# Optimization experiments

Measured on AMD Instinct MI355X. Metric: run time of the kernel, lower is better.

The kernel has to match this reference:

```python
import jax, jax.numpy as jnp
import numpy as np
from jax import lax

B, N, C = 4, 3072, 512
SAMPLE_RATIO = 0.25
CLUSTER_NUM = int(np.ceil(N * SAMPLE_RATIO))  # 768, static (mask=None, no 'r')
K = 5  # self.k, since k <= cluster_num


def setup_inputs() -> dict:
    key = jax.random.key(0)
    k1, = jax.random.split(key, 1)
    x = jax.random.normal(k1, (B, N, C), dtype=jnp.float32)
    # idx_token starts as identity mapping per batch (standard TCFormer init)
    idx_token = jnp.tile(jnp.arange(N, dtype=jnp.int32)[None, :], (B, 1))
    agg_weight = jnp.ones((B, N, 1), dtype=jnp.float32)
    return {"x": x, "idx_token": idx_token, "agg_weight": agg_weight}


def _cluster_dpc_knn(x):
    # runs under no_grad in torch -> stop_gradient here
    xs = lax.stop_gradient(x).astype(jnp.float32)
    sq = jnp.sum(xs * xs, axis=-1)  # [B,N]
    d2 = sq[:, :, None] + sq[:, None, :] - 2.0 * jnp.einsum('bnc,bmc->bnm', xs, xs)
    dist = jnp.sqrt(jnp.maximum(d2, 0.0)) / jnp.sqrt(jnp.float32(C))  # cdist / C**0.5
    # k nearest (smallest) distances
    neg_nearest, _ = lax.top_k(-dist, K)
    dist_nearest = -neg_nearest  # [B,N,K]
    density = jnp.exp(-jnp.mean(dist_nearest ** 2, axis=-1))
    density = density + jax.random.uniform(jax.random.key(42), density.shape, dtype=density.dtype) * 1e-6
    mask = (density[:, None, :] > density[:, :, None]).astype(x.dtype)  # [B,N,N]
    dist_max = jnp.max(dist.reshape(B, -1), axis=-1)[:, None, None]
    dist_min = jnp.min(dist * mask + dist_max * (1.0 - mask), axis=-1)  # [B,N]
    score = dist_min * density
    _, index_down = lax.top_k(score, CLUSTER_NUM)  # [B,cluster]
    # gather rows of dist at cluster centers, assign each token to nearest center
    dmat = jnp.take_along_axis(dist, index_down[:, :, None], axis=1)  # [B,cluster,N]
    idx_cluster = jnp.argmin(dmat, axis=1).astype(jnp.int32)  # [B,N]
    # force centers to map to their own cluster id
    idx_cluster = idx_cluster.at[jnp.arange(B)[:, None], index_down].set(
        jnp.broadcast_to(jnp.arange(CLUSTER_NUM, dtype=jnp.int32)[None, :], (B, CLUSTER_NUM)))
    return idx_cluster


def reference(x, idx_token, agg_weight):
    idx_cluster = _cluster_dpc_knn(x)
    # merge_tokens
    token_weight = jnp.ones((B, N, 1), dtype=x.dtype)
    idx = idx_cluster + jnp.arange(B, dtype=jnp.int32)[:, None] * CLUSTER_NUM  # [B,N]
    idx_flat = idx.reshape(-1)
    all_weight = jax.ops.segment_sum(token_weight.reshape(-1), idx_flat,
                                     num_segments=B * CLUSTER_NUM) + 1e-6  # [B*cluster]
    norm_weight = token_weight / all_weight[idx_flat].reshape(B, N, 1)  # [B,N,1]
    x_merged = jax.ops.segment_sum((x * norm_weight).reshape(B * N, C), idx_flat,
                                   num_segments=B * CLUSTER_NUM).reshape(B, CLUSTER_NUM, C)
    idx_token_new = jnp.take_along_axis(idx_cluster, idx_token, axis=1)  # [B,N]
    weight_t = jnp.take_along_axis(norm_weight, idx_token[:, :, None], axis=1)  # [B,N,1]
    agg_weight_new = agg_weight * weight_t
    return x_merged, agg_weight_new, idx_token_new, idx_cluster
```

## Files before the change

### kernel.cpp

```cpp
#include <hip/hip_runtime.h>
#include <math.h>
#include <float.h>

constexpr int B  = 4;
constexpr int N  = 3072;
constexpr int C  = 512;
constexpr int CL = 768;

typedef unsigned short u16;
typedef __attribute__((ext_vector_type(8))) short s16x8;
typedef __attribute__((ext_vector_type(4))) float f32x4;

__device__ __forceinline__ unsigned rotl32(unsigned v, int d) { return (v << d) | (v >> (32 - d)); }

__device__ inline void threefry2x32(unsigned k0, unsigned k1, unsigned c0, unsigned c1,
                                    unsigned& o0, unsigned& o1) {
  unsigned ks0 = k0, ks1 = k1, ks2 = 0x1BD11BDAu ^ k0 ^ k1;
  unsigned x0 = c0 + ks0, x1 = c1 + ks1;
#define TF_RND(r) { x0 += x1; x1 = rotl32(x1, (r)); x1 ^= x0; }
  TF_RND(13) TF_RND(15) TF_RND(26) TF_RND(6)  x0 += ks1; x1 += ks2 + 1u;
  TF_RND(17) TF_RND(29) TF_RND(16) TF_RND(24) x0 += ks2; x1 += ks0 + 2u;
  TF_RND(13) TF_RND(15) TF_RND(26) TF_RND(6)  x0 += ks0; x1 += ks1 + 3u;
  TF_RND(17) TF_RND(29) TF_RND(16) TF_RND(24) x0 += ks1; x1 += ks2 + 4u;
  TF_RND(13) TF_RND(15) TF_RND(26) TF_RND(6)  x0 += ks2; x1 += ks0 + 5u;
#undef TF_RND
  o0 = x0; o1 = x1;
}

__device__ inline float jax_uniform_bn(int f) {
  constexpr int HALF = (B * N) / 2;
  unsigned o0, o1, bits;
  if (f < HALF) { threefry2x32(0u, 42u, (unsigned)f, (unsigned)(f + HALF), o0, o1); bits = o0; }
  else          { threefry2x32(0u, 42u, (unsigned)(f - HALF), (unsigned)f, o0, o1); bits = o1; }
  return __uint_as_float((bits >> 9) | 0x3f800000u) - 1.0f;
}

__global__ void k_init(int* counts, unsigned long long* packed) {
  int g = blockIdx.x * 256 + threadIdx.x;
  packed[g] = ~0ull;
  if (g < B * CL) counts[g] = 0;
}

__global__ __launch_bounds__(64) void k_sq(const float* __restrict__ x, float* __restrict__ sq) {
  int row = blockIdx.x;
  int lane = threadIdx.x;
  const float* xr = x + (size_t)row * C;
  float s = 0.f;
  for (int c = lane * 4; c < C; c += 256) {
    float4 v = *(const float4*)(xr + c);
    s += v.x * v.x + v.y * v.y + v.z * v.z + v.w * v.w;
  }
  for (int o = 32; o > 0; o >>= 1) s += __shfl_down(s, o, 64);
  if (lane == 0) sq[row] = s;
}

__device__ __forceinline__ u16 bf16rn(float f) {
  unsigned u = __float_as_uint(f);
  unsigned r = u + 0x7FFFu + ((u >> 16) & 1u);
  return (u16)(r >> 16);
}
__device__ __forceinline__ float bf16tof(u16 h) {
  return __uint_as_float(((unsigned)h) << 16);
}

__global__ void k_split(const float* __restrict__ x, u16* __restrict__ xhi, u16* __restrict__ xlo) {
  int g = (blockIdx.x * 256 + threadIdx.x) * 4;
  float4 v = *(const float4*)(x + g);
  u16 h0 = bf16rn(v.x), h1 = bf16rn(v.y), h2 = bf16rn(v.z), h3 = bf16rn(v.w);
  u16 l0 = bf16rn(v.x - bf16tof(h0));
  u16 l1 = bf16rn(v.y - bf16tof(h1));
  u16 l2 = bf16rn(v.z - bf16tof(h2));
  u16 l3 = bf16rn(v.w - bf16tof(h3));
  uint2 hp, lp;
  hp.x = (unsigned)h0 | ((unsigned)h1 << 16); hp.y = (unsigned)h2 | ((unsigned)h3 << 16);
  lp.x = (unsigned)l0 | ((unsigned)l1 << 16); lp.y = (unsigned)l2 | ((unsigned)l3 << 16);
  *(uint2*)(xhi + g) = hp;
  *(uint2*)(xlo + g) = lp;
}

__device__ __forceinline__ void ins5b(float t[5], float v) {
  float c = v;
  float n;
  n = fminf(t[0], c); c = fmaxf(t[0], c); t[0] = n;
  n = fminf(t[1], c); c = fmaxf(t[1], c); t[1] = n;
  n = fminf(t[2], c); c = fmaxf(t[2], c); t[2] = n;
  n = fminf(t[3], c); c = fmaxf(t[3], c); t[3] = n;
  t[4] = fminf(t[4], c);
}

constexpr int NT3 = N / 128;
constexpr int NTILE3 = NT3 * (NT3 + 1) / 2;

__global__ __launch_bounds__(256) void k_distm(const u16* __restrict__ xhi, const u16* __restrict__ xlo,
                                               const float* __restrict__ sq,
                                               float* __restrict__ distbuf,
                                               float* __restrict__ part5, int b0) {
  constexpr int ASTR = 40;
  __shared__ __align__(16) char smem[40960];
  u16* sAh = (u16*)smem;
  u16* sAl = sAh + 128 * ASTR;
  u16* sBh = sAl + 128 * ASTR;
  u16* sBl = sBh + 128 * ASTR;

  int bl = blockIdx.y, b = b0 + bl;
  int idx = blockIdx.x;
  int ti = 0, rem = idx;
  while (rem >= NT3 - ti) { rem -= NT3 - ti; ++ti; }
  int tj = ti + rem;
  int i0 = ti * 128, j0 = tj * 128;
  bool do_mirror = (ti != tj);

  const float* sqb = sq + (size_t)b * N;
  float* dist = distbuf + (size_t)bl * N * N;

  int tid = threadIdx.x;
  int srow = tid >> 1, shalf = (tid & 1) * 16;
  const u16* gAh = xhi + ((size_t)b * N + i0 + srow) * C + shalf;
  const u16* gAl = xlo + ((size_t)b * N + i0 + srow) * C + shalf;
  const u16* gBh = xhi + ((size_t)b * N + j0 + srow) * C + shalf;
  const u16* gBl = xlo + ((size_t)b * N + j0 + srow) * C + shalf;
  int wofs = srow * ASTR + shalf;

  int lane = tid & 63, w = tid >> 6;
  int wr = (w >> 1) * 64, wc = (w & 1) * 64;
  int l15 = lane & 15, l4 = lane >> 4;

  f32x4 acc[4][4];
#pragma unroll
  for (int rt = 0; rt < 4; ++rt)
#pragma unroll
    for (int ct = 0; ct < 4; ++ct)
#pragma unroll
      for (int e = 0; e < 4; ++e) acc[rt][ct][e] = 0.f;

  uint4 p0 = *(const uint4*)gAh, p1 = *(const uint4*)(gAh + 8);
  uint4 p2 = *(const uint4*)gAl, p3 = *(const uint4*)(gAl + 8);
  uint4 p4 = *(const uint4*)gBh, p5 = *(const uint4*)(gBh + 8);
  uint4 p6 = *(const uint4*)gBl, p7 = *(const uint4*)(gBl + 8);

  for (int k0 = 0; k0 < C; k0 += 32) {
    *(uint4*)&sAh[wofs] = p0; *(uint4*)&sAh[wofs + 8] = p1;
    *(uint4*)&sAl[wofs] = p2; *(uint4*)&sAl[wofs + 8] = p3;
    *(uint4*)&sBh[wofs] = p4; *(uint4*)&sBh[wofs + 8] = p5;
    *(uint4*)&sBl[wofs] = p6; *(uint4*)&sBl[wofs + 8] = p7;
    __syncthreads();
    int kn = k0 + 32;
    if (kn < C) {
      p0 = *(const uint4*)(gAh + kn); p1 = *(const uint4*)(gAh + kn + 8);
      p2 = *(const uint4*)(gAl + kn); p3 = *(const uint4*)(gAl + kn + 8);
      p4 = *(const uint4*)(gBh + kn); p5 = *(const uint4*)(gBh + kn + 8);
      p6 = *(const uint4*)(gBl + kn); p7 = *(const uint4*)(gBl + kn + 8);
    }
    s16x8 ah[4], al[4];
#pragma unroll
    for (int rt = 0; rt < 4; ++rt) {
      int ro = (wr + rt * 16 + l15) * ASTR + l4 * 8;
      ah[rt] = *(const s16x8*)&sAh[ro];
      al[rt] = *(const s16x8*)&sAl[ro];
    }
#pragma unroll
    for (int ct = 0; ct < 4; ++ct) {
      int co = (wc + ct * 16 + l15) * ASTR + l4 * 8;
      s16x8 bh = *(const s16x8*)&sBh[co];
      s16x8 bl = *(const s16x8*)&sBl[co];
#pragma unroll
      for (int rt = 0; rt < 4; ++rt) {
        acc[rt][ct] = __builtin_amdgcn_mfma_f32_16x16x32_bf16(ah[rt], bh, acc[rt][ct], 0, 0, 0);
        acc[rt][ct] = __builtin_amdgcn_mfma_f32_16x16x32_bf16(ah[rt], bl, acc[rt][ct], 0, 0, 0);
        acc[rt][ct] = __builtin_amdgcn_mfma_f32_16x16x32_bf16(al[rt], bh, acc[rt][ct], 0, 0, 0);
      }
    }
    __syncthreads();
  }

  const float SQC = 22.627416997969522f;
  float sqi[4][4], sqj[4];
#pragma unroll
  for (int rt = 0; rt < 4; ++rt)
#pragma unroll
    for (int r = 0; r < 4; ++r) sqi[rt][r] = sqb[i0 + wr + rt * 16 + l4 * 4 + r];
#pragma unroll
  for (int ct = 0; ct < 4; ++ct) sqj[ct] = sqb[j0 + wc + ct * 16 + l15];

#pragma unroll
  for (int rt = 0; rt < 4; ++rt)
#pragma unroll
    for (int ct = 0; ct < 4; ++ct)
#pragma unroll
      for (int r = 0; r < 4; ++r) {
        float d2 = fmaxf(sqi[rt][r] + sqj[ct] - 2.0f * acc[rt][ct][r], 0.0f);
        acc[rt][ct][r] = sqrtf(d2) / SQC;
      }

  constexpr int TSTR = 76;
  float* sT = (float*)smem + w * (32 * TSTR);

  float t5A[5] = {FLT_MAX, FLT_MAX, FLT_MAX, FLT_MAX, FLT_MAX};
  float mxA = 0.f;

#pragma unroll
  for (int p = 0; p < 2; ++p) {
#pragma unroll
    for (int cth = 0; cth < 2; ++cth) {
      int ct = p * 2 + cth;
      int cl = cth * 16 + l15;
#pragma unroll
      for (int rt = 0; rt < 4; ++rt)
#pragma unroll
        for (int r = 0; r < 4; ++r)
          sT[cl * TSTR + rt * 16 + l4 * 4 + r] = acc[rt][ct][r];
    }
    {
      int g4 = lane & 7, rbase = lane >> 3;
#pragma unroll
      for (int it = 0; it < 8; ++it) {
        int rl = it * 8 + rbase;
        float4 v = make_float4(sT[(4 * g4 + 0) * TSTR + rl],
                               sT[(4 * g4 + 1) * TSTR + rl],
                               sT[(4 * g4 + 2) * TSTR + rl],
                               sT[(4 * g4 + 3) * TSTR + rl]);
        *(float4*)(dist + (size_t)(i0 + wr + rl) * N + j0 + wc + p * 32 + 4 * g4) = v;
      }
    }
    if (do_mirror) {
      int cg = lane >> 4, rq = lane & 15;
#pragma unroll
      for (int cc = 0; cc < 8; ++cc) {
        int c = cc * 4 + cg;
        float4 v = *(const float4*)&sT[c * TSTR + rq * 4];
        *(float4*)(dist + (size_t)(j0 + wc + p * 32 + c) * N + i0 + wr + rq * 4) = v;
      }
    }
    for (int c = 0; c < 32; ++c) {
      float v = sT[c * TSTR + lane];
      mxA = fmaxf(mxA, v);
      ins5b(t5A, v);
    }
    if (do_mirror) {
      int cl = lane & 31, half = lane >> 5;
      float t5B[5] = {FLT_MAX, FLT_MAX, FLT_MAX, FLT_MAX, FLT_MAX};
      float mxB = 0.f;
      for (int k = 0; k < 32; ++k) {
        float v = sT[cl * TSTR + half * 32 + k];
        mxB = fmaxf(mxB, v);
        ins5b(t5B, v);
      }
      mxB = fmaxf(mxB, __shfl_xor(mxB, 32, 64));
      float o0 = __shfl_xor(t5B[0], 32, 64);
      float o1 = __shfl_xor(t5B[1], 32, 64);
      float o2 = __shfl_xor(t5B[2], 32, 64);
      float o3 = __shfl_xor(t5B[3], 32, 64);
      float o4 = __shfl_xor(t5B[4], 32, 64);
      ins5b(t5B, o0); ins5b(t5B, o1); ins5b(t5B, o2); ins5b(t5B, o3); ins5b(t5B, o4);
      if (half == 0) {
        int rowB = j0 + wc + p * 32 + cl;
        int slotB = ti * 2 + (wr >> 6);
        float* dst = part5 + (((size_t)bl * 48 + slotB) * 6) * N + rowB;
        dst[0] = t5B[0]; dst[(size_t)N] = t5B[1]; dst[2 * (size_t)N] = t5B[2];
        dst[3 * (size_t)N] = t5B[3]; dst[4 * (size_t)N] = t5B[4]; dst[5 * (size_t)N] = mxB;
      }
    }
  }
  {
    int rowA = i0 + wr + lane;
    int slotA = tj * 2 + (wc >> 6);
    float* dst = part5 + (((size_t)bl * 48 + slotA) * 6) * N + rowA;
    dst[0] = t5A[0]; dst[(size_t)N] = t5A[1]; dst[2 * (size_t)N] = t5A[2];
    dst[3 * (size_t)N] = t5A[3]; dst[4 * (size_t)N] = t5A[4]; dst[5 * (size_t)N] = mxA;
  }
}

__global__ __launch_bounds__(256) void k_dens(const float* __restrict__ part5,
                                              float* __restrict__ density,
                                              float* __restrict__ rowmax, int b0) {
  int g = blockIdx.x * 256 + threadIdx.x;
  int bl = g / N, r = g % N;
  int b = b0 + bl;
  const float* base = part5 + (size_t)bl * 48 * 6 * N + r;
  float t5[5] = {FLT_MAX, FLT_MAX, FLT_MAX, FLT_MAX, FLT_MAX};
  float mx = 0.f;
  for (int s = 0; s < 48; ++s) {
    const float* sp = base + (size_t)s * 6 * N;
    ins5b(t5, sp[0]);
    ins5b(t5, sp[(size_t)N]);
    ins5b(t5, sp[2 * (size_t)N]);
    ins5b(t5, sp[3 * (size_t)N]);
    ins5b(t5, sp[4 * (size_t)N]);
    mx = fmaxf(mx, sp[5 * (size_t)N]);
  }
  float sum = t5[0] * t5[0] + t5[1] * t5[1] + t5[2] * t5[2] + t5[3] * t5[3] + t5[4] * t5[4];
  density[b * N + r] = expf(-(sum / 5.0f)) + jax_uniform_bn(b * N + r) * 1e-6f;
  rowmax[b * N + r] = mx;
}

__global__ __launch_bounds__(1024) void k_dmax(const float* __restrict__ rowmax,
                                               float* __restrict__ distmax) {
  __shared__ float red[16];
  int b = blockIdx.x;
  int tid = threadIdx.x;
  const float* rb = rowmax + (size_t)b * N;
  float mx = 0.f;
  for (int j = tid; j < N; j += 1024) mx = fmaxf(mx, rb[j]);
#pragma unroll
  for (int m = 1; m < 64; m <<= 1) mx = fmaxf(mx, __shfl_xor(mx, m, 64));
  if ((tid & 63) == 0) red[tid >> 6] = mx;
  __syncthreads();
  if (tid == 0) {
    float r = red[0];
#pragma unroll
    for (int q = 1; q < 16; ++q) r = fmaxf(r, red[q]);
    distmax[b] = r;
  }
}

__global__ __launch_bounds__(256) void k_maskmin(const float* __restrict__ distbuf,
                                                 const float* __restrict__ density,
                                                 const float* __restrict__ distmax,
                                                 float* __restrict__ score, int b0) {
  __shared__ float sd[N];
  int tid = threadIdx.x;
  int wv = tid >> 6, lane = tid & 63;
  int i = blockIdx.x * 4 + wv;
  int bl = blockIdx.y, b = b0 + bl;
  const float* db = density + (size_t)b * N;
  for (int j = tid * 4; j < N; j += 1024) *(float4*)(sd + j) = *(const float4*)(db + j);
  __syncthreads();
  float di = sd[i];
  float dmax = distmax[b];
  const float* row = distbuf + ((size_t)bl * N + i) * N;
  float mn = dmax;
#pragma unroll
  for (int it = 0; it < N / 256; ++it) {
    int j = it * 256 + lane * 4;
    float4 v = *(const float4*)(row + j);
    float4 d = *(const float4*)(sd + j);
    mn = fminf(mn, (d.x > di) ? v.x : dmax);
    mn = fminf(mn, (d.y > di) ? v.y : dmax);
    mn = fminf(mn, (d.z > di) ? v.z : dmax);
    mn = fminf(mn, (d.w > di) ? v.w : dmax);
  }
#pragma unroll
  for (int m = 1; m < 64; m <<= 1) mn = fminf(mn, __shfl_xor(mn, m, 64));
  if (lane == 0) score[b * N + i] = mn * di;
}

__global__ __launch_bounds__(256) void k_rank(const float* __restrict__ score,
                                              int* __restrict__ index_down,
                                              int* __restrict__ rank, int b0) {
  __shared__ float ssc[N];
  int tid = threadIdx.x;
  int wv = tid >> 6, lane = tid & 63;
  int i = blockIdx.x * 4 + wv;
  int b = b0 + blockIdx.y;
  const float* sb = score + (size_t)b * N;
  for (int j = tid * 4; j < N; j += 1024) *(float4*)(ssc + j) = *(const float4*)(sb + j);
  __syncthreads();
  float si = ssc[i];
  int cnt = 0;
#pragma unroll
  for (int it = 0; it < N / 256; ++it) {
    int j = it * 256 + lane * 4;
    float4 v = *(const float4*)(ssc + j);
    cnt += (v.x > si) || (v.x == si && (j + 0) < i);
    cnt += (v.y > si) || (v.y == si && (j + 1) < i);
    cnt += (v.z > si) || (v.z == si && (j + 2) < i);
    cnt += (v.w > si) || (v.w == si && (j + 3) < i);
  }
#pragma unroll
  for (int m = 1; m < 64; m <<= 1) cnt += __shfl_xor(cnt, m, 64);
  if (lane == 0) {
    rank[b * N + i] = (cnt < CL) ? cnt : -1;
    if (cnt < CL) index_down[b * CL + cnt] = i;
  }
}

__global__ __launch_bounds__(256) void k_assign_part(const float* __restrict__ distbuf,
                                                     const int* __restrict__ index_down,
                                                     unsigned long long* __restrict__ packed, int b0) {
  constexpr int RCH = CL / 8;
  __shared__ int sid[RCH];
  int bl = blockIdx.z, b = b0 + bl;
  int r0 = blockIdx.y * RCH;
  int tid = threadIdx.x;
  for (int r = tid; r < RCH; r += 256) sid[r] = index_down[b * CL + r0 + r];
  __syncthreads();
  int j = blockIdx.x * 256 + tid;
  const float* base = distbuf + (size_t)bl * N * N;
  float best = FLT_MAX; int bestr = 0;
#pragma unroll 8
  for (int r = 0; r < RCH; ++r) {
    float d = base[(size_t)sid[r] * N + j];
    if (d < best) { best = d; bestr = r0 + r; }
  }
  unsigned long long key = ((unsigned long long)__float_as_uint(best) << 32) | (unsigned)bestr;
  atomicMin(&packed[b * N + j], key);
}

__global__ void k_assign_fin2(const unsigned long long* __restrict__ packed,
                              const int* __restrict__ rank,
                              int* __restrict__ idx_cluster, int* __restrict__ counts) {
  int g = blockIdx.x * 256 + threadIdx.x;
  int b = g / N;
  int r = rank[g];
  int cl = (r >= 0) ? r : (int)(unsigned)(packed[g] & 0xffffffffull);
  idx_cluster[g] = cl;
  atomicAdd(&counts[b * CL + cl], 1);
}

__global__ __launch_bounds__(1024) void k_scan(const int* __restrict__ counts,
                                               int* __restrict__ offsets, int* __restrict__ cursor) {
  constexpr int T = B * CL;
  __shared__ int sm[T];
  int tid = threadIdx.x;
  for (int p = tid; p < T; p += 1024) sm[p] = counts[p];
  __syncthreads();
  for (int off = 1; off < T; off <<= 1) {
    int v[3]; int n = 0;
    for (int p = tid; p < T; p += 1024) { v[n++] = (p >= off) ? sm[p - off] : 0; }
    __syncthreads();
    n = 0;
    for (int p = tid; p < T; p += 1024) { sm[p] += v[n++]; }
    __syncthreads();
  }
  for (int p = tid; p < T; p += 1024) {
    int e = sm[p] - counts[p];
    offsets[p] = e; cursor[p] = e;
  }
}

__global__ void k_fill(const int* __restrict__ idx_cluster, int* __restrict__ cursor,
                       int* __restrict__ members) {
  int g = blockIdx.x * 256 + threadIdx.x;
  int b = g / N, i = g % N;
  int seg = b * CL + idx_cluster[g];
  int pos = atomicAdd(&cursor[seg], 1);
  members[pos] = i;
}

__global__ __launch_bounds__(128) void k_gather(const float* __restrict__ x, const int* __restrict__ members,
                                                const int* __restrict__ offsets, const int* __restrict__ counts,
                                                float* __restrict__ out0) {
  int seg = blockIdx.x;
  int b = seg / CL;
  int cnt = counts[seg], off = offsets[seg];
  float nw = 1.0f / ((float)cnt + 1e-6f);
  int c = threadIdx.x * 4;
  const float* xb = x + (size_t)b * N * C;
  float4 acc = make_float4(0.f, 0.f, 0.f, 0.f);
  for (int m = 0; m < cnt; ++m) {
    int tok = members[off + m];
    float4 v = *(const float4*)(xb + (size_t)tok * C + c);
    acc.x += v.x * nw; acc.y += v.y * nw; acc.z += v.z * nw; acc.w += v.w * nw;
  }
  *(float4*)(out0 + (size_t)seg * C + c) = acc;
}

__global__ void k_final(const float* __restrict__ agg_weight, const int* __restrict__ idx_token,
                        const int* __restrict__ idx_cluster, const int* __restrict__ counts,
                        float* __restrict__ out1, float* __restrict__ out2, float* __restrict__ out3) {
  int g = blockIdx.x * 256 + threadIdx.x;
  int b = g / N;
  int it = idx_token[g];
  int clt = idx_cluster[b * N + it];
  float nwt = 1.0f / ((float)counts[b * CL + clt] + 1e-6f);
  out1[g] = agg_weight[g] * nwt;
  out2[g] = (float)clt;
  out3[g] = (float)idx_cluster[g];
}

extern "C" void kernel_launch(void* const* d_in, const int* in_sizes, int n_in,
                              void* d_out, int out_size, void* d_ws, size_t ws_size,
                              hipStream_t stream) {
  const float* x          = (const float*)d_in[0];
  const int*   idx_token  = (const int*)d_in[1];
  const float* agg_weight = (const float*)d_in[2];

  float* out0 = (float*)d_out;
  float* out1 = out0 + (size_t)B * CL * C;
  float* out2 = out1 + (size_t)B * N;
  float* out3 = out2 + (size_t)B * N;

  char* w = (char*)d_ws;
  auto carve = [&](size_t bytes) { char* p = w; w += (bytes + 255) & ~(size_t)255; return p; };
  float*    sq         = (float*)carve((size_t)B * N * 4);
  float*    density    = (float*)carve((size_t)B * N * 4);
  float*    score      = (float*)carve((size_t)B * N * 4);
  float*    rowmax     = (float*)carve((size_t)B * N * 4);
  float*    distmax    = (float*)carve((size_t)B * 4);
  int*      index_down = (int*)carve((size_t)B * CL * 4);
  int*      rank       = (int*)carve((size_t)B * N * 4);
  int*      idx_clus   = (int*)carve((size_t)B * N * 4);
  int*      counts     = (int*)carve((size_t)B * CL * 4);
  int*      offsets    = (int*)carve((size_t)B * CL * 4);
  int*      cursor     = (int*)carve((size_t)B * CL * 4);
  int*      members    = (int*)carve((size_t)B * N * 4);
  unsigned long long* packed = (unsigned long long*)carve((size_t)B * N * 8);
  u16*      xhi        = (u16*)carve((size_t)B * N * C * 2);
  u16*      xlo        = (u16*)carve((size_t)B * N * C * 2);
  float*    part5      = (float*)carve((size_t)B * 48 * 6 * N * 4);
  size_t used = (size_t)(w - (char*)d_ws);
  size_t per  = (size_t)N * N * 4;
  int nb_max = (ws_size > used) ? (int)((ws_size - used) / per) : 0;
  if (nb_max < 1) nb_max = 1;
  if (nb_max > B) nb_max = B;
  float* distbuf = (float*)w;

  k_init<<<(B * N) / 256, 256, 0, stream>>>(counts, packed);
  k_sq<<<B * N, 64, 0, stream>>>(x, sq);
  k_split<<<(B * N * C) / 1024, 256, 0, stream>>>(x, xhi, xlo);

  for (int b0 = 0; b0 < B; b0 += nb_max) {
    int nb = (B - b0 < nb_max) ? (B - b0) : nb_max;
    k_distm<<<dim3(NTILE3, nb), 256, 0, stream>>>(xhi, xlo, sq, distbuf, part5, b0);
    k_dens<<<(nb * N) / 256, 256, 0, stream>>>(part5, density, rowmax, b0);
    k_dmax<<<nb, 1024, 0, stream>>>(rowmax + (size_t)b0 * N, distmax + b0);
    k_maskmin<<<dim3(N / 4, nb), 256, 0, stream>>>(distbuf, density, distmax, score, b0);
    k_rank<<<dim3(N / 4, nb), 256, 0, stream>>>(score, index_down, rank, b0);
    k_assign_part<<<dim3(N / 256, 8, nb), 256, 0, stream>>>(distbuf, index_down, packed, b0);
  }

  k_assign_fin2<<<(B * N) / 256, 256, 0, stream>>>(packed, rank, idx_clus, counts);
  k_scan<<<1, 1024, 0, stream>>>(counts, offsets, cursor);
  k_fill<<<(B * N) / 256, 256, 0, stream>>>(idx_clus, cursor, members);
  k_gather<<<B * CL, 128, 0, stream>>>(x, members, offsets, counts, out0);
  k_final<<<(B * N) / 256, 256, 0, stream>>>(agg_weight, idx_token, idx_clus, counts, out1, out2, out3);
}
```

Before: 307.1 us.

## Recompute distances via GEMM instead of materializing the full distance matrix

The full B×N×N fp32 distance matrix is no longer written to global memory. Masked-min and cluster-assignment stages now recompute distances with split-bf16 MFMA GEMMs: a second symmetric GEMM pass does the density-masked min, and a gathered center×token GEMM does the argmin. The sq, split and init kernels are fused into one prep kernel, and the per-batch chunking loop is removed. This trades roughly 150MB of dist writes and rereads for extra tensor-core work. It also adds partial-min buffers and an extra reduction kernel.

```diff
diff --git a/kernel.cpp b/kernel.cpp
--- a/kernel.cpp
+++ b/kernel.cpp
@@ -35,47 +35,45 @@
   return __uint_as_float((bits >> 9) | 0x3f800000u) - 1.0f;
 }
 
-__global__ void k_init(int* counts, unsigned long long* packed) {
-  int g = blockIdx.x * 256 + threadIdx.x;
-  packed[g] = ~0ull;
-  if (g < B * CL) counts[g] = 0;
-}
-
-__global__ __launch_bounds__(64) void k_sq(const float* __restrict__ x, float* __restrict__ sq) {
+__device__ __forceinline__ u16 bf16rn(float f) {
+  unsigned u = __float_as_uint(f);
+  unsigned r = u + 0x7FFFu + ((u >> 16) & 1u);
+  return (u16)(r >> 16);
+}
+__device__ __forceinline__ float bf16tof(u16 h) {
+  return __uint_as_float(((unsigned)h) << 16);
+}
+
+__global__ __launch_bounds__(64) void k_prep(const float* __restrict__ x, float* __restrict__ sq,
+                                             u16* __restrict__ xhi, u16* __restrict__ xlo,
+                                             int* __restrict__ counts,
+                                             unsigned long long* __restrict__ packed) {
   int row = blockIdx.x;
   int lane = threadIdx.x;
   const float* xr = x + (size_t)row * C;
+  u16* hr = xhi + (size_t)row * C;
+  u16* lr = xlo + (size_t)row * C;
   float s = 0.f;
   for (int c = lane * 4; c < C; c += 256) {
     float4 v = *(const float4*)(xr + c);
     s += v.x * v.x + v.y * v.y + v.z * v.z + v.w * v.w;
+    u16 h0 = bf16rn(v.x), h1 = bf16rn(v.y), h2 = bf16rn(v.z), h3 = bf16rn(v.w);
+    u16 l0 = bf16rn(v.x - bf16tof(h0));
+    u16 l1 = bf16rn(v.y - bf16tof(h1));
+    u16 l2 = bf16rn(v.z - bf16tof(h2));
+    u16 l3 = bf16rn(v.w - bf16tof(h3));
+    uint2 hp, lp;
+    hp.x = (unsigned)h0 | ((unsigned)h1 << 16); hp.y = (unsigned)h2 | ((unsigned)h3 << 16);
+    lp.x = (unsigned)l0 | ((unsigned)l1 << 16); lp.y = (unsigned)l2 | ((unsigned)l3 << 16);
+    *(uint2*)(hr + c) = hp;
+    *(uint2*)(lr + c) = lp;
   }
   for (int o = 32; o > 0; o >>= 1) s += __shfl_down(s, o, 64);
-  if (lane == 0) sq[row] = s;
-}
-
-__device__ __forceinline__ u16 bf16rn(float f) {
-  unsigned u = __float_as_uint(f);
-  unsigned r = u + 0x7FFFu + ((u >> 16) & 1u);
-  return (u16)(r >> 16);
-}
-__device__ __forceinline__ float bf16tof(u16 h) {
-  return __uint_as_float(((unsigned)h) << 16);
-}
-
-__global__ void k_split(const float* __restrict__ x, u16* __restrict__ xhi, u16* __restrict__ xlo) {
-  int g = (blockIdx.x * 256 + threadIdx.x) * 4;
-  float4 v = *(const float4*)(x + g);
-  u16 h0 = bf16rn(v.x), h1 = bf16rn(v.y), h2 = bf16rn(v.z), h3 = bf16rn(v.w);
-  u16 l0 = bf16rn(v.x - bf16tof(h0));
-  u16 l1 = bf16rn(v.y - bf16tof(h1));
-  u16 l2 = bf16rn(v.z - bf16tof(h2));
-  u16 l3 = bf16rn(v.w - bf16tof(h3));
-  uint2 hp, lp;
-  hp.x = (unsigned)h0 | ((unsigned)h1 << 16); hp.y = (unsigned)h2 | ((unsigned)h3 << 16);
-  lp.x = (unsigned)l0 | ((unsigned)l1 << 16); lp.y = (unsigned)l2 | ((unsigned)l3 << 16);
-  *(uint2*)(xhi + g) = hp;
-  *(uint2*)(xlo + g) = lp;
+  if (lane == 0) {
+    sq[row] = s;
+    packed[row] = ~0ull;
+    if (row < B * CL) counts[row] = 0;
+  }
 }
 
 __device__ __forceinline__ void ins5b(float t[5], float v) {
@@ -91,10 +89,9 @@
 constexpr int NT3 = N / 128;
 constexpr int NTILE3 = NT3 * (NT3 + 1) / 2;
 
-__global__ __launch_bounds__(256) void k_distm(const u16* __restrict__ xhi, const u16* __restrict__ xlo,
+__global__ __launch_bounds__(256) void k_gemm1(const u16* __restrict__ xhi, const u16* __restrict__ xlo,
                                                const float* __restrict__ sq,
-                                               float* __restrict__ distbuf,
-                                               float* __restrict__ part5, int b0) {
+                                               float* __restrict__ part5) {
   constexpr int ASTR = 40;
   __shared__ __align__(16) char smem[40960];
   u16* sAh = (u16*)smem;
@@ -102,7 +99,7 @@
   u16* sBh = sAl + 128 * ASTR;
   u16* sBl = sBh + 128 * ASTR;
 
-  int bl = blockIdx.y, b = b0 + bl;
+  int b = blockIdx.y;
   int idx = blockIdx.x;
   int ti = 0, rem = idx;
   while (rem >= NT3 - ti) { rem -= NT3 - ti; ++ti; }
@@ -111,7 +108,6 @@
   bool do_mirror = (ti != tj);
 
   const float* sqb = sq + (size_t)b * N;
-  float* dist = distbuf + (size_t)bl * N * N;
 
   int tid = threadIdx.x;
   int srow = tid >> 1, shalf = (tid & 1) * 16;
@@ -210,27 +206,6 @@
         for (int r = 0; r < 4; ++r)
           sT[cl * TSTR + rt * 16 + l4 * 4 + r] = acc[rt][ct][r];
     }
-    {
-      int g4 = lane & 7, rbase = lane >> 3;
-#pragma unroll
-      for (int it = 0; it < 8; ++it) {
-        int rl = it * 8 + rbase;
-        float4 v = make_float4(sT[(4 * g4 + 0) * TSTR + rl],
-                               sT[(4 * g4 + 1) * TSTR + rl],
-                               sT[(4 * g4 + 2) * TSTR + rl],
-                               sT[(4 * g4 + 3) * TSTR + rl]);
-        *(float4*)(dist + (size_t)(i0 + wr + rl) * N + j0 + wc + p * 32 + 4 * g4) = v;
-      }
-    }
-    if (do_mirror) {
-      int cg = lane >> 4, rq = lane & 15;
-#pragma unroll
-      for (int cc = 0; cc < 8; ++cc) {
-        int c = cc * 4 + cg;
-        float4 v = *(const float4*)&sT[c * TSTR + rq * 4];
-        *(float4*)(dist + (size_t)(j0 + wc + p * 32 + c) * N + i0 + wr + rq * 4) = v;
-      }
-    }
     for (int c = 0; c < 32; ++c) {
       float v = sT[c * TSTR + lane];
       mxA = fmaxf(mxA, v);
@@ -255,7 +230,7 @@
       if (half == 0) {
         int rowB = j0 + wc + p * 32 + cl;
         int slotB = ti * 2 + (wr >> 6);
-        float* dst = part5 + (((size_t)bl * 48 + slotB) * 6) * N + rowB;
+        float* dst = part5 + (((size_t)b * 48 + slotB) * 6) * N + rowB;
         dst[0] = t5B[0]; dst[(size_t)N] = t5B[1]; dst[2 * (size_t)N] = t5B[2];
         dst[3 * (size_t)N] = t5B[3]; dst[4 * (size_t)N] = t5B[4]; dst[5 * (size_t)N] = mxB;
       }
@@ -264,7 +239,7 @@
   {
     int rowA = i0 + wr + lane;
     int slotA = tj * 2 + (wc >> 6);
-    float* dst = part5 + (((size_t)bl * 48 + slotA) * 6) * N + rowA;
+    float* dst = part5 + (((size_t)b * 48 + slotA) * 6) * N + rowA;
     dst[0] = t5A[0]; dst[(size_t)N] = t5A[1]; dst[2 * (size_t)N] = t5A[2];
     dst[3 * (size_t)N] = t5A[3]; dst[4 * (size_t)N] = t5A[4]; dst[5 * (size_t)N] = mxA;
   }
@@ -272,11 +247,10 @@
 
 __global__ __launch_bounds__(256) void k_dens(const float* __restrict__ part5,
                                               float* __restrict__ density,
-                                              float* __restrict__ rowmax, int b0) {
+                                              float* __restrict__ rowmax) {
   int g = blockIdx.x * 256 + threadIdx.x;
-  int bl = g / N, r = g % N;
-  int b = b0 + bl;
-  const float* base = part5 + (size_t)bl * 48 * 6 * N + r;
+  int b = g / N, r = g % N;
+  const float* base = part5 + (size_t)b * 48 * 6 * N + r;
   float t5[5] = {FLT_MAX, FLT_MAX, FLT_MAX, FLT_MAX, FLT_MAX};
   float mx = 0.f;
   for (int s = 0; s < 48; ++s) {
@@ -289,8 +263,8 @@
     mx = fmaxf(mx, sp[5 * (size_t)N]);
   }
   float sum = t5[0] * t5[0] + t5[1] * t5[1] + t5[2] * t5[2] + t5[3] * t5[3] + t5[4] * t5[4];
-  density[b * N + r] = expf(-(sum / 5.0f)) + jax_uniform_bn(b * N + r) * 1e-6f;
-  rowmax[b * N + r] = mx;
+  density[g] = expf(-(sum / 5.0f)) + jax_uniform_bn(g) * 1e-6f;
+  rowmax[g] = mx;
 }
 
 __global__ __launch_bounds__(1024) void k_dmax(const float* __restrict__ rowmax,
@@ -313,45 +287,177 @@
   }
 }
 
-__global__ __launch_bounds__(256) void k_maskmin(const float* __restrict__ distbuf,
-                                                 const float* __restrict__ density,
-                                                 const float* __restrict__ distmax,
-                                                 float* __restrict__ score, int b0) {
-  __shared__ float sd[N];
+__global__ __launch_bounds__(256) void k_gemm2(const u16* __restrict__ xhi, const u16* __restrict__ xlo,
+                                               const float* __restrict__ sq,
+                                               const float* __restrict__ density,
+                                               float* __restrict__ partmin) {
+  constexpr int ASTR = 40;
+  __shared__ __align__(16) char smem[40960];
+  u16* sAh = (u16*)smem;
+  u16* sAl = sAh + 128 * ASTR;
+  u16* sBh = sAl + 128 * ASTR;
+  u16* sBl = sBh + 128 * ASTR;
+
+  int b = blockIdx.y;
+  int idx = blockIdx.x;
+  int ti = 0, rem = idx;
+  while (rem >= NT3 - ti) { rem -= NT3 - ti; ++ti; }
+  int tj = ti + rem;
+  int i0 = ti * 128, j0 = tj * 128;
+  bool do_mirror = (ti != tj);
+
+  const float* sqb = sq + (size_t)b * N;
+
   int tid = threadIdx.x;
-  int wv = tid >> 6, lane = tid & 63;
-  int i = blockIdx.x * 4 + wv;
-  int bl = blockIdx.y, b = b0 + bl;
+  int srow = tid >> 1, shalf = (tid & 1) * 16;
+  const u16* gAh = xhi + ((size_t)b * N + i0 + srow) * C + shalf;
+  const u16* gAl = xlo + ((size_t)b * N + i0 + srow) * C + shalf;
+  const u16* gBh = xhi + ((size_t)b * N + j0 + srow) * C + shalf;
+  const u16* gBl = xlo + ((size_t)b * N + j0 + srow) * C + shalf;
+  int wofs = srow * ASTR + shalf;
+
+  int lane = tid & 63, w = tid >> 6;
+  int wr = (w >> 1) * 64, wc = (w & 1) * 64;
+  int l15 = lane & 15, l4 = lane >> 4;
+
+  f32x4 acc[4][4];
+#pragma unroll
+  for (int rt = 0; rt < 4; ++rt)
+#pragma unroll
+    for (int ct = 0; ct < 4; ++ct)
+#pragma unroll
+      for (int e = 0; e < 4; ++e) acc[rt][ct][e] = 0.f;
+
+  uint4 p0 = *(const uint4*)gAh, p1 = *(const uint4*)(gAh + 8);
+  uint4 p2 = *(const uint4*)gAl, p3 = *(const uint4*)(gAl + 8);
+  uint4 p4 = *(const uint4*)gBh, p5 = *(const uint4*)(gBh + 8);
+  uint4 p6 = *(const uint4*)gBl, p7 = *(const uint4*)(gBl + 8);
+
+  for (int k0 = 0; k0 < C; k0 += 32) {
+    *(uint4*)&sAh[wofs] = p0; *(uint4*)&sAh[wofs + 8] = p1;
+    *(uint4*)&sAl[wofs] = p2; *(uint4*)&sAl[wofs + 8] = p3;
+    *(uint4*)&sBh[wofs] = p4; *(uint4*)&sBh[wofs + 8] = p5;
+    *(uint4*)&sBl[wofs] = p6; *(uint4*)&sBl[wofs + 8] = p7;
+    __syncthreads();
+    int kn = k0 + 32;
+    if (kn < C) {
+      p0 = *(const uint4*)(gAh + kn); p1 = *(const uint4*)(gAh + kn + 8);
+      p2 = *(const uint4*)(gAl + kn); p3 = *(const uint4*)(gAl + kn + 8);
+      p4 = *(const uint4*)(gBh + kn); p5 = *(const uint4*)(gBh + kn + 8);
+      p6 = *(const uint4*)(gBl + kn); p7 = *(const uint4*)(gBl + kn + 8);
+    }
+    s16x8 ah[4], al[4];
+#pragma unroll
+    for (int rt = 0; rt < 4; ++rt) {
+      int ro = (wr + rt * 16 + l15) * ASTR + l4 * 8;
+      ah[rt] = *(const s16x8*)&sAh[ro];
+      al[rt] = *(const s16x8*)&sAl[ro];
+    }
+#pragma unroll
+    for (int ct = 0; ct < 4; ++ct) {
+      int co = (wc + ct * 16 + l15) * ASTR + l4 * 8;
+      s16x8 bh = *(const s16x8*)&sBh[co];
+      s16x8 bl = *(const s16x8*)&sBl[co];
+#pragma unroll
+      for (int rt = 0; rt < 4; ++rt) {
+        acc[rt][ct] = __builtin_amdgcn_mfma_f32_16x16x32_bf16(ah[rt], bh, acc[rt][ct], 0, 0, 0);
+        acc[rt][ct] = __builtin_amdgcn_mfma_f32_16x16x32_bf16(ah[rt], bl, acc[rt][ct], 0, 0, 0);
+        acc[rt][ct] = __builtin_amdgcn_mfma_f32_16x16x32_bf16(al[rt], bh, acc[rt][ct], 0, 0, 0);
+      }
+    }
+    __syncthreads();
+  }
+
+  const float SQC = 22.627416997969522f;
+  float sqi[4][4], sqj[4];
+#pragma unroll
+  for (int rt = 0; rt < 4; ++rt)
+#pragma unroll
+    for (int r = 0; r < 4; ++r) sqi[rt][r] = sqb[i0 + wr + rt * 16 + l4 * 4 + r];
+#pragma unroll
+  for (int ct = 0; ct < 4; ++ct) sqj[ct] = sqb[j0 + wc + ct * 16 + l15];
+
+#pragma unroll
+  for (int rt = 0; rt < 4; ++rt)
+#pragma unroll
+    for (int ct = 0; ct < 4; ++ct)
+#pragma unroll
+      for (int r = 0; r < 4; ++r) {
+        float d2 = fmaxf(sqi[rt][r] + sqj[ct] - 2.0f * acc[rt][ct][r], 0.0f);
+        acc[rt][ct][r] = sqrtf(d2) / SQC;
+      }
+
+  constexpr int TSTR = 76;
+  float* sT  = (float*)smem + w * (32 * TSTR);
+  float* sDc = (float*)smem + 4 * (32 * TSTR) + w * 128;
+  float* sDr = sDc + 64;
   const float* db = density + (size_t)b * N;
-  for (int j = tid * 4; j < N; j += 1024) *(float4*)(sd + j) = *(const float4*)(db + j);
-  __syncthreads();
-  float di = sd[i];
-  float dmax = distmax[b];
-  const float* row = distbuf + ((size_t)bl * N + i) * N;
-  float mn = dmax;
-#pragma unroll
-  for (int it = 0; it < N / 256; ++it) {
-    int j = it * 256 + lane * 4;
-    float4 v = *(const float4*)(row + j);
-    float4 d = *(const float4*)(sd + j);
-    mn = fminf(mn, (d.x > di) ? v.x : dmax);
-    mn = fminf(mn, (d.y > di) ? v.y : dmax);
-    mn = fminf(mn, (d.z > di) ? v.z : dmax);
-    mn = fminf(mn, (d.w > di) ? v.w : dmax);
-  }
-#pragma unroll
-  for (int m = 1; m < 64; m <<= 1) mn = fminf(mn, __shfl_xor(mn, m, 64));
-  if (lane == 0) score[b * N + i] = mn * di;
+  float dureg = db[i0 + wr + lane];
+  float dcreg = db[j0 + wc + lane];
+  sDr[lane] = dureg;
+  sDc[lane] = dcreg;
+
+  float mnA = FLT_MAX;
+#pragma unroll
+  for (int p = 0; p < 2; ++p) {
+#pragma unroll
+    for (int cth = 0; cth < 2; ++cth) {
+      int ct = p * 2 + cth;
+      int cl = cth * 16 + l15;
+#pragma unroll
+      for (int rt = 0; rt < 4; ++rt)
+#pragma unroll
+        for (int r = 0; r < 4; ++r)
+          sT[cl * TSTR + rt * 16 + l4 * 4 + r] = acc[rt][ct][r];
+    }
+    for (int c = 0; c < 32; ++c) {
+      float v = sT[c * TSTR + lane];
+      float dc = sDc[p * 32 + c];
+      mnA = fminf(mnA, (dc > dureg) ? v : FLT_MAX);
+    }
+    if (do_mirror) {
+      int cl = lane & 31, half = lane >> 5;
+      float dv = sDc[p * 32 + cl];
+      float mnB = FLT_MAX;
+      for (int k = 0; k < 32; ++k) {
+        float du = sDr[half * 32 + k];
+        float v = sT[cl * TSTR + half * 32 + k];
+        mnB = fminf(mnB, (du > dv) ? v : FLT_MAX);
+      }
+      mnB = fminf(mnB, __shfl_xor(mnB, 32, 64));
+      if (half == 0) {
+        int rowB = j0 + wc + p * 32 + cl;
+        int slotB = ti * 2 + (wr >> 6);
+        partmin[((size_t)b * 48 + slotB) * N + rowB] = mnB;
+      }
+    }
+  }
+  {
+    int rowA = i0 + wr + lane;
+    int slotA = tj * 2 + (wc >> 6);
+    partmin[((size_t)b * 48 + slotA) * N + rowA] = mnA;
+  }
+}
+
+__global__ void k_score(const float* __restrict__ partmin, const float* __restrict__ density,
+                        const float* __restrict__ distmax, float* __restrict__ score) {
+  int g = blockIdx.x * 256 + threadIdx.x;
+  int b = g / N, r = g % N;
+  float mn = distmax[b];
+  const float* base = partmin + (size_t)b * 48 * N + r;
+#pragma unroll
+  for (int s = 0; s < 48; ++s) mn = fminf(mn, base[(size_t)s * N]);
+  score[g] = mn * density[g];
 }
 
 __global__ __launch_bounds__(256) void k_rank(const float* __restrict__ score,
                                               int* __restrict__ index_down,
-                                              int* __restrict__ rank, int b0) {
+                                              int* __restrict__ rank) {
   __shared__ float ssc[N];
   int tid = threadIdx.x;
   int wv = tid >> 6, lane = tid & 63;
   int i = blockIdx.x * 4 + wv;
-  int b = b0 + blockIdx.y;
+  int b = blockIdx.y;
   const float* sb = score + (size_t)b * N;
   for (int j = tid * 4; j < N; j += 1024) *(float4*)(ssc + j) = *(const float4*)(sb + j);
   __syncthreads();
@@ -374,26 +480,118 @@
   }
 }
 
-__global__ __launch_bounds__(256) void k_assign_part(const float* __restrict__ distbuf,
-                                                     const int* __restrict__ index_down,
-                                                     unsigned long long* __restrict__ packed, int b0) {
-  constexpr int RCH = CL / 8;
-  __shared__ int sid[RCH];
-  int bl = blockIdx.z, b = b0 + bl;
-  int r0 = blockIdx.y * RCH;
+__global__ __launch_bounds__(256) void k_assign2(const u16* __restrict__ xhi, const u16* __restrict__ xlo,
+                                                 const float* __restrict__ sq,
+                                                 const int* __restrict__ index_down,
+                                                 unsigned long long* __restrict__ packed) {
+  constexpr int ASTR = 40;
+  __shared__ __align__(16) char smem[40960];
+  u16* sAh = (u16*)smem;
+  u16* sAl = sAh + 128 * ASTR;
+  u16* sBh = sAl + 128 * ASTR;
+  u16* sBl = sBh + 128 * ASTR;
+
+  int jt = blockIdx.x;
+  int rt_blk = blockIdx.y;
+  int b = blockIdx.z;
+  int j0 = jt * 128, r0 = rt_blk * 128;
+
+  const float* sqb = sq + (size_t)b * N;
+  const int* idb = index_down + (size_t)b * CL;
+
   int tid = threadIdx.x;
-  for (int r = tid; r < RCH; r += 256) sid[r] = index_down[b * CL + r0 + r];
-  __syncthreads();
-  int j = blockIdx.x * 256 + tid;
-  const float* base = distbuf + (size_t)bl * N * N;
-  float best = FLT_MAX; int bestr = 0;
-#pragma unroll 8
-  for (int r = 0; r < RCH; ++r) {
-    float d = base[(size_t)sid[r] * N + j];
-    if (d < best) { best = d; bestr = r0 + r; }
-  }
-  unsigned long long key = ((unsigned long long)__float_as_uint(best) << 32) | (unsigned)bestr;
-  atomicMin(&packed[b * N + j], key);
+  int srow = tid >> 1, shalf = (tid & 1) * 16;
+  int cid = idb[r0 + srow];
+  const u16* gAh = xhi + ((size_t)b * N + cid) * C + shalf;
+  const u16* gAl = xlo + ((size_t)b * N + cid) * C + shalf;
+  const u16* gBh = xhi + ((size_t)b * N + j0 + srow) * C + shalf;
+  const u16* gBl = xlo + ((size_t)b * N + j0 + srow) * C + shalf;
+  int wofs = srow * ASTR + shalf;
+
+  int lane = tid & 63, w = tid >> 6;
+  int wr = (w >> 1) * 64, wc = (w & 1) * 64;
+  int l15 = lane & 15, l4 = lane >> 4;
+
+  f32x4 acc[4][4];
+#pragma unroll
+  for (int rt = 0; rt < 4; ++rt)
+#pragma unroll
+    for (int ct = 0; ct < 4; ++ct)
+#pragma unroll
+      for (int e = 0; e < 4; ++e) acc[rt][ct][e] = 0.f;
+
+  uint4 p0 = *(const uint4*)gAh, p1 = *(const uint4*)(gAh + 8);
+  uint4 p2 = *(const uint4*)gAl, p3 = *(const uint4*)(gAl + 8);
+  uint4 p4 = *(const uint4*)gBh, p5 = *(const uint4*)(gBh + 8);
+  uint4 p6 = *(const uint4*)gBl, p7 = *(const uint4*)(gBl + 8);
+
+  for (int k0 = 0; k0 < C; k0 += 32) {
+    *(uint4*)&sAh[wofs] = p0; *(uint4*)&sAh[wofs + 8] = p1;
+    *(uint4*)&sAl[wofs] = p2; *(uint4*)&sAl[wofs + 8] = p3;
+    *(uint4*)&sBh[wofs] = p4; *(uint4*)&sBh[wofs + 8] = p5;
+    *(uint4*)&sBl[wofs] = p6; *(uint4*)&sBl[wofs + 8] = p7;
+    __syncthreads();
+    int kn = k0 + 32;
+    if (kn < C) {
+      p0 = *(const uint4*)(gAh + kn); p1 = *(const uint4*)(gAh + kn + 8);
+      p2 = *(const uint4*)(gAl + kn); p3 = *(const uint4*)(gAl + kn + 8);
+      p4 = *(const uint4*)(gBh + kn); p5 = *(const uint4*)(gBh + kn + 8);
+      p6 = *(const uint4*)(gBl + kn); p7 = *(const uint4*)(gBl + kn + 8);
+    }
+    s16x8 ah[4], al[4];
+#pragma unroll
+    for (int rt = 0; rt < 4; ++rt) {
+      int ro = (wr + rt * 16 + l15) * ASTR + l4 * 8;
+      ah[rt] = *(const s16x8*)&sAh[ro];
+      al[rt] = *(const s16x8*)&sAl[ro];
+    }
+#pragma unroll
+    for (int ct = 0; ct < 4; ++ct) {
+      int co = (wc + ct * 16 + l15) * ASTR + l4 * 8;
+      s16x8 bh = *(const s16x8*)&sBh[co];
+      s16x8 bl = *(const s16x8*)&sBl[co];
+#pragma unroll
+      for (int rt = 0; rt < 4; ++rt) {
+        acc[rt][ct] = __builtin_amdgcn_mfma_f32_16x16x32_bf16(ah[rt], bh, acc[rt][ct], 0, 0, 0);
+        acc[rt][ct] = __builtin_amdgcn_mfma_f32_16x16x32_bf16(ah[rt], bl, acc[rt][ct], 0, 0, 0);
+        acc[rt][ct] = __builtin_amdgcn_mfma_f32_16x16x32_bf16(al[rt], bh, acc[rt][ct], 0, 0, 0);
+      }
+    }
+    __syncthreads();
+  }
+
+  const float SQC = 22.627416997969522f;
+  float sqi[4][4];
+  int cidx[4][4];
+#pragma unroll
+  for (int rt = 0; rt < 4; ++rt)
+#pragma unroll
+    for (int r = 0; r < 4; ++r) {
+      int rr = r0 + wr + rt * 16 + l4 * 4 + r;
+      cidx[rt][r] = rr;
+      sqi[rt][r] = sqb[idb[rr]];
+    }
+  float sqj[4];
+#pragma unroll
+  for (int ct = 0; ct < 4; ++ct) sqj[ct] = sqb[j0 + wc + ct * 16 + l15];
+
+#pragma unroll
+  for (int ct = 0; ct < 4; ++ct) {
+    unsigned long long best = ~0ull;
+#pragma unroll
+    for (int rt = 0; rt < 4; ++rt)
+#pragma unroll
+      for (int r = 0; r < 4; ++r) {
+        float d2 = fmaxf(sqi[rt][r] + sqj[ct] - 2.0f * acc[rt][ct][r], 0.0f);
+        float d = sqrtf(d2) / SQC;
+        unsigned long long key = ((unsigned long long)__float_as_uint(d) << 32) | (unsigned)cidx[rt][r];
+        best = (key < best) ? key : best;
+      }
+    unsigned long long o;
+    o = __shfl_xor(best, 16, 64); best = (o < best) ? o : best;
+    o = __shfl_xor(best, 32, 64); best = (o < best) ? o : best;
+    if (l4 == 0) atomicMin(&packed[(size_t)b * N + j0 + wc + ct * 16 + l15], best);
+  }
 }
 
 __global__ void k_assign_fin2(const unsigned long long* __restrict__ packed,
@@ -498,27 +696,17 @@
   u16*      xhi        = (u16*)carve((size_t)B * N * C * 2);
   u16*      xlo        = (u16*)carve((size_t)B * N * C * 2);
   float*    part5      = (float*)carve((size_t)B * 48 * 6 * N * 4);
-  size_t used = (size_t)(w - (char*)d_ws);
-  size_t per  = (size_t)N * N * 4;
-  int nb_max = (ws_size > used) ? (int)((ws_size - used) / per) : 0;
-  if (nb_max < 1) nb_max = 1;
-  if (nb_max > B) nb_max = B;
-  float* distbuf = (float*)w;
-
-  k_init<<<(B * N) / 256, 256, 0, stream>>>(counts, packed);
-  k_sq<<<B * N, 64, 0, stream>>>(x, sq);
-  k_split<<<(B * N * C) / 1024, 256, 0, stream>>>(x, xhi, xlo);
-
-  for (int b0 = 0; b0 < B; b0 += nb_max) {
-    int nb = (B - b0 < nb_max) ? (B - b0) : nb_max;
-    k_distm<<<dim3(NTILE3, nb), 256, 0, stream>>>(xhi, xlo, sq, distbuf, part5, b0);
-    k_dens<<<(nb * N) / 256, 256, 0, stream>>>(part5, density, rowmax, b0);
-    k_dmax<<<nb, 1024, 0, stream>>>(rowmax + (size_t)b0 * N, distmax + b0);
-    k_maskmin<<<dim3(N / 4, nb), 256, 0, stream>>>(distbuf, density, distmax, score, b0);
-    k_rank<<<dim3(N / 4, nb), 256, 0, stream>>>(score, index_down, rank, b0);
-    k_assign_part<<<dim3(N / 256, 8, nb), 256, 0, stream>>>(distbuf, index_down, packed, b0);
-  }
-
+  float*    partmin    = (float*)carve((size_t)B * 48 * N * 4);
+  (void)ws_size;
+
+  k_prep<<<B * N, 64, 0, stream>>>(x, sq, xhi, xlo, counts, packed);
+  k_gemm1<<<dim3(NTILE3, B), 256, 0, stream>>>(xhi, xlo, sq, part5);
+  k_dens<<<(B * N) / 256, 256, 0, stream>>>(part5, density, rowmax);
+  k_dmax<<<B, 1024, 0, stream>>>(rowmax, distmax);
+  k_gemm2<<<dim3(NTILE3, B), 256, 0, stream>>>(xhi, xlo, sq, density, partmin);
+  k_score<<<(B * N) / 256, 256, 0, stream>>>(partmin, density, distmax, score);
+  k_rank<<<dim3(N / 4, B), 256, 0, stream>>>(score, index_down, rank);
+  k_assign2<<<dim3(NT3, CL / 128, B), 256, 0, stream>>>(xhi, xlo, sq, index_down, packed);
   k_assign_fin2<<<(B * N) / 256, 256, 0, stream>>>(packed, rank, idx_clus, counts);
   k_scan<<<1, 1024, 0, stream>>>(counts, offsets, cursor);
   k_fill<<<(B * N) / 256, 256, 0, stream>>>(idx_clus, cursor, members);
```

Result: slower. 394.5 us (+28.4%).
